# Performance work log

Measured on AMD Instinct MI355X. Metric: run time of the kernel, lower is better.

## Reference

```python
import jax, jax.numpy as jnp
import numpy as np

GAMMA = 0.01      # rbf gamma (init kwarg)
C = 10            # n_classes (len(nv))
NV = 500          # support vectors per class (equal segments)
# all (i, j) class pairs with i < j, in the original nested-loop order
PAIRS = np.array([(i, j) for i in range(C) for j in range(i + 1, C)], dtype=np.int32)
I_IDX = jnp.asarray(PAIRS[:, 0])  # [45]
J_IDX = jnp.asarray(PAIRS[:, 1])  # [45]


def setup_inputs() -> dict:
    key = jax.random.key(0)
    k1, k2, k3, k4 = jax.random.split(key, 4)
    x = jax.random.normal(k1, (8192, 256), dtype=jnp.float32)
    sv = jax.random.normal(k2, (5000, 256), dtype=jnp.float32)
    a = jax.random.normal(k3, (C - 1, 5000), dtype=jnp.float32) * 0.1  # dual coefs
    b = jax.random.normal(k4, (45,), dtype=jnp.float32) * 0.1          # intercepts per pair
    return {"x": x, "sv": sv, "a": a, "b": b}


def reference(x, sv, a, b):
    # RBF kernel matrix: k[n, s] = exp(-gamma * ||x_n - sv_s||^2)
    x_norm = jnp.sum(x * x, axis=1)[:, None]            # [N, 1]
    sv_norm = jnp.sum(sv * sv, axis=1)[None, :]         # [1, SV]
    k = jnp.exp(-GAMMA * (x_norm + sv_norm) + 2.0 * GAMMA * (x @ sv.T))  # [N, SV]

    N = x.shape[0]
    kr = k.reshape(N, C, NV)           # per-class SV segments
    ar = a.reshape(C - 1, C, NV)       # dual coef rows, segmented the same way
    # T[n, r, c] = sum_m a[r, segment c, m] * k[n, segment c, m]
    # (fuses every inner Python loop of the original into one contraction)
    T = jnp.einsum('ncm,rcm->nrc', kr, ar)              # [N, C-1, C]

    # decision for pair (i, j): a[i, seg j] . k_seg_j + a[j-1, seg i] . k_seg_i + b
    c = T[:, I_IDX, J_IDX] + T[:, J_IDX - 1, I_IDX] + b[None, :]  # [N, 45]

    # pairwise voting: winner i if c > 0 else j; class id = mode of votes
    votes = jnp.where(c > 0, I_IDX[None, :], J_IDX[None, :])      # [N, 45] int32
    counts = jnp.sum(jax.nn.one_hot(votes, C, dtype=jnp.float32), axis=1)  # [N, C]
    # argmax picks the smallest class index on ties, matching torch.mode
    class_ids = jnp.argmax(counts, axis=1).astype(jnp.int32)
    return (class_ids, class_ids)
```

## Files before the change

kernel.cpp:

```cpp
#include <hip/hip_runtime.h>
#include <hip/hip_fp16.h>
#include <cmath>


#define GAMMA 0.01f
constexpr int N  = 8192;
constexpr int D  = 256;
constexpr int S  = 5000;
constexpr int C  = 10;
constexpr int NV = 500;
constexpr int R  = 9;
constexpr int SPAD = 5120;

constexpr int ROW_BLOCKS = (N + S) / 4;
constexpr int A_BLOCKS   = (16 * SPAD) / 256;

typedef _Float16 f16x8 __attribute__((ext_vector_type(8)));
typedef _Float16 f16x4 __attribute__((ext_vector_type(4)));
typedef float    f32x4 __attribute__((ext_vector_type(4)));

__device__ __forceinline__ void gload16(const void* g, void* l) {
    __builtin_amdgcn_global_load_lds(
        (const __attribute__((address_space(1))) void*)g,
        (__attribute__((address_space(3))) void*)l, 16, 0, 0);
}

__global__ __launch_bounds__(256) void prep_kernel(const float* __restrict__ x,
                                                   const float* __restrict__ sv,
                                                   const float* __restrict__ a,
                                                   _Float16* __restrict__ xh,
                                                   _Float16* __restrict__ xl,
                                                   _Float16* __restrict__ sh,
                                                   _Float16* __restrict__ sl,
                                                   float* __restrict__ xn,
                                                   _Float16* __restrict__ ah,
                                                   _Float16* __restrict__ al,
                                                   float* __restrict__ svnp) {
    if (blockIdx.x >= ROW_BLOCKS) {
        int idx = (blockIdx.x - ROW_BLOCKS) * 256 + threadIdx.x;
        int r = idx / SPAD, col = idx - r * SPAD;
        int cls = col >> 9, j = col & 511;
        int s = cls * NV + ((j < NV) ? j : NV - 1);
        float av = (r < R && j < NV) ? a[(size_t)r * S + s] : 0.0f;
        _Float16 h = (_Float16)av;
        ah[idx] = h;
        al[idx] = (_Float16)((av - (float)h) * 4096.0f);
        return;
    }
    int gid  = blockIdx.x * blockDim.x + threadIdx.x;
    int wid  = gid >> 6;
    int lane = gid & 63;
    bool isx = wid < N;
    int  r   = isx ? wid : wid - N;
    const float* row = isx ? (x + (size_t)r * D) : (sv + (size_t)r * D);
    float4 v = reinterpret_cast<const float4*>(row)[lane];
    float s = v.x * v.x + v.y * v.y + v.z * v.z + v.w * v.w;
#pragma unroll
    for (int off = 32; off > 0; off >>= 1) s += __shfl_xor(s, off, 64);
    float vv[4] = {v.x, v.y, v.z, v.w};
    f16x4 h, l;
#pragma unroll
    for (int k = 0; k < 4; ++k) {
        _Float16 hi = (_Float16)vv[k];
        h[k] = hi;
        l[k] = (_Float16)((vv[k] - (float)hi) * 4096.0f);
    }
    size_t o = (size_t)r * D + lane * 4;
    *(f16x4*)((isx ? xh : sh) + o) = h;
    *(f16x4*)((isx ? xl : sl) + o) = l;
    if (lane == 0) {
        if (isx) {
            xn[r] = s;
        } else {
            int cls = r / NV, j = r - cls * NV;
            svnp[cls * 512 + j] = s;
            if (j == NV - 1)
                for (int p = NV; p < 512; ++p) svnp[cls * 512 + p] = s;
        }
    }
}

__global__ __launch_bounds__(256, 3) void svc_gemm(const _Float16* __restrict__ xh,
                                                   const _Float16* __restrict__ xl,
                                                   const _Float16* __restrict__ sh,
                                                   const _Float16* __restrict__ sl,
                                                   const _Float16* __restrict__ ahp,
                                                   const _Float16* __restrict__ alp,
                                                   const float* __restrict__ xnorm,
                                                   const float* __restrict__ svnp,
                                                   float* __restrict__ T) {
    __shared__ _Float16 SVs[2][2][128 * 32];
    __shared__ _Float16 Xs[2][2][64 * 32];

    const int tid  = threadIdx.x;
    const int n0   = blockIdx.x * 64;
    const int cls  = blockIdx.y;
    const int w    = tid >> 6;
    const int lane = tid & 63;
    const int wm   = w >> 1;
    const int wn   = w & 1;
    const int lx   = lane & 15;
    const int quad = lane >> 4;

    float xnr[2];
#pragma unroll
    for (int nt = 0; nt < 2; ++nt)
        xnr[nt] = xnorm[n0 + wn * 32 + nt * 16 + lx];

    int svoff[4], xoff[2];
#pragma unroll
    for (int mt = 0; mt < 4; ++mt) {
        int row = wm * 64 + mt * 16 + lx;
        svoff[mt] = row * 32 + ((quad - (row >> 1)) & 3) * 8;
    }
#pragma unroll
    for (int nt = 0; nt < 2; ++nt) {
        int row = wn * 32 + nt * 16 + lx;
        xoff[nt] = row * 32 + ((quad - (row >> 1)) & 3) * 8;
    }

    const int arow = tid >> 2, ag = tid & 3;
    const int sg   = (ag + (arow >> 1)) & 3;
    const int segend = cls * NV + NV - 1;
    const int ldsw = w * 512;

    auto stage = [&](int ph, int buf) {
        const int ch = ph >> 3, kb = ph & 7;
        const size_t koff = (size_t)(kb * 32 + sg * 8);
        const size_t goX  = (size_t)(n0 + arow) * D + koff;
        gload16(xh + goX, &Xs[buf][0][ldsw]);
        gload16(xl + goX, &Xs[buf][1][ldsw]);
        const int svbase = cls * NV + ch * 128;
        int svr0 = svbase + arow;      if (svr0 > segend) svr0 = segend;
        int svr1 = svbase + arow + 64; if (svr1 > segend) svr1 = segend;
        const size_t go0 = (size_t)svr0 * D + koff;
        const size_t go1 = (size_t)svr1 * D + koff;
        gload16(sh + go0, &SVs[buf][0][ldsw]);
        gload16(sl + go0, &SVs[buf][1][ldsw]);
        gload16(sh + go1, &SVs[buf][0][2048 + ldsw]);
        gload16(sl + go1, &SVs[buf][1][2048 + ldsw]);
    };

    f32x4 accM[4][2], accC[4][2];
#pragma unroll
    for (int mt = 0; mt < 4; ++mt)
#pragma unroll
        for (int nt = 0; nt < 2; ++nt) {
            accM[mt][nt] = (f32x4){0.f, 0.f, 0.f, 0.f};
            accC[mt][nt] = (f32x4){0.f, 0.f, 0.f, 0.f};
        }
    f32x4 accO[2], accOC[2];
#pragma unroll
    for (int nt = 0; nt < 2; ++nt) {
        accO[nt]  = (f32x4){0.f, 0.f, 0.f, 0.f};
        accOC[nt] = (f32x4){0.f, 0.f, 0.f, 0.f};
    }

    stage(0, 0);

    for (int ph = 0; ph < 32; ++ph) {
        const int buf = ph & 1;
        if (ph < 31) {
            stage(ph + 1, buf ^ 1);
            asm volatile("s_waitcnt vmcnt(6)" ::: "memory");
        } else {
            asm volatile("s_waitcnt vmcnt(0)" ::: "memory");
        }
        __builtin_amdgcn_s_barrier();
        asm volatile("" ::: "memory");

        f16x8 Am[2][4], Bx[2][2];
#pragma unroll
        for (int mt = 0; mt < 4; ++mt) {
            Am[0][mt] = *(const f16x8*)(&SVs[buf][0][svoff[mt]]);
            Am[1][mt] = *(const f16x8*)(&SVs[buf][1][svoff[mt]]);
        }
#pragma unroll
        for (int nt = 0; nt < 2; ++nt) {
            Bx[0][nt] = *(const f16x8*)(&Xs[buf][0][xoff[nt]]);
            Bx[1][nt] = *(const f16x8*)(&Xs[buf][1][xoff[nt]]);
        }
        __builtin_amdgcn_s_setprio(1);
#pragma unroll
        for (int mt = 0; mt < 4; ++mt)
#pragma unroll
            for (int nt = 0; nt < 2; ++nt) {
                accM[mt][nt] = __builtin_amdgcn_mfma_f32_16x16x32_f16(
                    Am[0][mt], Bx[0][nt], accM[mt][nt], 0, 0, 0);
                accC[mt][nt] = __builtin_amdgcn_mfma_f32_16x16x32_f16(
                    Am[0][mt], Bx[1][nt], accC[mt][nt], 0, 0, 0);
                accC[mt][nt] = __builtin_amdgcn_mfma_f32_16x16x32_f16(
                    Am[1][mt], Bx[0][nt], accC[mt][nt], 0, 0, 0);
            }
        __builtin_amdgcn_s_setprio(0);

        if ((ph & 7) == 7) {
            const int ch = ph >> 3;
            const int mbase = cls * 512 + ch * 128 + wm * 64;
#pragma unroll
            for (int mt = 0; mt < 4; ++mt) {
                const size_t ao = (size_t)lx * SPAD + mbase + mt * 16 + quad * 4;
                f16x4 afh = *(const f16x4*)(ahp + ao);
                f16x4 afl = *(const f16x4*)(alp + ao);
                float4 sn4 = *(const float4*)(svnp + mbase + mt * 16 + quad * 4);
#pragma unroll
                for (int nt = 0; nt < 2; ++nt) {
                    f16x4 bh, bl;
#pragma unroll
                    for (int reg = 0; reg < 4; ++reg) {
                        float dot = accM[mt][nt][reg]
                                  + accC[mt][nt][reg] * (1.0f / 4096.0f);
                        float e  = fmaf(2.0f * GAMMA, dot,
                                        -GAMMA * (xnr[nt] + sn4[reg]));
                        float kv = __expf(e);
                        _Float16 h = (_Float16)kv;
                        bh[reg] = h;
                        bl[reg] = (_Float16)((kv - (float)h) * 4096.0f);
                    }
                    accO[nt]  = __builtin_amdgcn_mfma_f32_16x16x16f16(
                        afh, bh, accO[nt], 0, 0, 0);
                    accOC[nt] = __builtin_amdgcn_mfma_f32_16x16x16f16(
                        afh, bl, accOC[nt], 0, 0, 0);
                    accOC[nt] = __builtin_amdgcn_mfma_f32_16x16x16f16(
                        afl, bh, accOC[nt], 0, 0, 0);
                    accM[mt][nt] = (f32x4){0.f, 0.f, 0.f, 0.f};
                    accC[mt][nt] = (f32x4){0.f, 0.f, 0.f, 0.f};
                }
            }
        }

        asm volatile("s_waitcnt lgkmcnt(0)" ::: "memory");
        __builtin_amdgcn_s_barrier();
        asm volatile("" ::: "memory");
    }

    float* scr = (float*)&SVs[0][0][0];
    if (wm == 0) {
#pragma unroll
        for (int nt = 0; nt < 2; ++nt)
#pragma unroll
            for (int reg = 0; reg < 4; ++reg) {
                int base = ((wn * 2 + nt) * 2) * 256 + (quad * 4 + reg) * 16 + lx;
                scr[base]       = accO[nt][reg];
                scr[base + 256] = accOC[nt][reg];
            }
    }
    __syncthreads();
    if (wm == 1) {
#pragma unroll
        for (int nt = 0; nt < 2; ++nt)
#pragma unroll
            for (int reg = 0; reg < 4; ++reg) {
                int r = quad * 4 + reg;
                if (r < R) {
                    int base = ((wn * 2 + nt) * 2) * 256 + r * 16 + lx;
                    float o  = accO[nt][reg]  + scr[base];
                    float oc = accOC[nt][reg] + scr[base + 256];
                    int n = n0 + wn * 32 + nt * 16 + lx;
                    T[(size_t)(r * 10 + cls) * N + n] = o + oc * (1.0f / 4096.0f);
                }
            }
    }
}

__global__ __launch_bounds__(256) void vote_kernel(const float* __restrict__ T,
                                                   const float* __restrict__ b,
                                                   int* __restrict__ out) {
    int n = blockIdx.x * blockDim.x + threadIdx.x;
    if (n >= N) return;
    float tv[90];
#pragma unroll
    for (int i = 0; i < 90; ++i) tv[i] = T[(size_t)i * N + n];
    int counts[C];
#pragma unroll
    for (int k = 0; k < C; ++k) counts[k] = 0;
    int p = 0;
#pragma unroll
    for (int i = 0; i < C; ++i) {
#pragma unroll
        for (int j = i + 1; j < C; ++j) {
            float c = tv[i * 10 + j] + tv[(j - 1) * 10 + i] + b[p];
            if (c > 0.f) counts[i]++; else counts[j]++;
            ++p;
        }
    }
    int best = 0;
#pragma unroll
    for (int k = 1; k < C; ++k)
        if (counts[k] > counts[best]) best = k;
    out[n]     = best;
    out[N + n] = best;
}

extern "C" void kernel_launch(void* const* d_in, const int* in_sizes, int n_in,
                              void* d_out, int out_size, void* d_ws, size_t ws_size,
                              hipStream_t stream) {
    const float* x  = (const float*)d_in[0];
    const float* sv = (const float*)d_in[1];
    const float* a  = (const float*)d_in[2];
    const float* b  = (const float*)d_in[3];
    int* out = (int*)d_out;

    char* wp = (char*)d_ws;
    _Float16* xh = (_Float16*)wp;  wp += (size_t)N * D * 2;
    _Float16* xl = (_Float16*)wp;  wp += (size_t)N * D * 2;
    _Float16* sh = (_Float16*)wp;  wp += (size_t)S * D * 2;
    _Float16* sl = (_Float16*)wp;  wp += (size_t)S * D * 2;
    float* xnorm  = (float*)wp;    wp += (size_t)N * 4;
    _Float16* ahp = (_Float16*)wp; wp += (size_t)16 * SPAD * 2;
    _Float16* alp = (_Float16*)wp; wp += (size_t)16 * SPAD * 2;
    float* svnp   = (float*)wp;    wp += (size_t)SPAD * 4;
    float* T      = (float*)wp;

    {
        prep_kernel<<<ROW_BLOCKS + A_BLOCKS, 256, 0, stream>>>(
            x, sv, a, xh, xl, sh, sl, xnorm, ahp, alp, svnp);
    }
    {
        dim3 grid(N / 64, C);
        svc_gemm<<<grid, 256, 0, stream>>>(xh, xl, sh, sl, ahp, alp,
                                           xnorm, svnp, T);
    }
    {
        vote_kernel<<<N / 256, 256, 0, stream>>>(T, b, out);
    }
}
```

Measured before the change: 164.6 us.

## Load X fragments directly into registers instead of staging through LDS

Removes the X tile from shared memory. Each wave now loads its own f16 hi/lo X fragments from global memory straight into registers, double-buffered across even and odd phases, while the SV tile still goes through LDS. The main loop is unrolled by two so each register buffer has a fixed name. This saves LDS traffic and capacity, which may allow more blocks per CU, but the two waves sharing an X slice now fetch it separately and the vmcnt accounting becomes more delicate.

```diff
diff --git a/kernel.cpp b/kernel.cpp
--- a/kernel.cpp
+++ b/kernel.cpp
@@ -90,7 +90,6 @@
                                                    const float* __restrict__ svnp,
                                                    float* __restrict__ T) {
     __shared__ _Float16 SVs[2][2][128 * 32];
-    __shared__ _Float16 Xs[2][2][64 * 32];
 
     const int tid  = threadIdx.x;
     const int n0   = blockIdx.x * 64;
@@ -107,16 +106,11 @@
     for (int nt = 0; nt < 2; ++nt)
         xnr[nt] = xnorm[n0 + wn * 32 + nt * 16 + lx];
 
-    int svoff[4], xoff[2];
+    int svoff[4];
 #pragma unroll
     for (int mt = 0; mt < 4; ++mt) {
         int row = wm * 64 + mt * 16 + lx;
         svoff[mt] = row * 32 + ((quad - (row >> 1)) & 3) * 8;
-    }
-#pragma unroll
-    for (int nt = 0; nt < 2; ++nt) {
-        int row = wn * 32 + nt * 16 + lx;
-        xoff[nt] = row * 32 + ((quad - (row >> 1)) & 3) * 8;
     }
 
     const int arow = tid >> 2, ag = tid & 3;
@@ -127,9 +121,6 @@
     auto stage = [&](int ph, int buf) {
         const int ch = ph >> 3, kb = ph & 7;
         const size_t koff = (size_t)(kb * 32 + sg * 8);
-        const size_t goX  = (size_t)(n0 + arow) * D + koff;
-        gload16(xh + goX, &Xs[buf][0][ldsw]);
-        gload16(xl + goX, &Xs[buf][1][ldsw]);
         const int svbase = cls * NV + ch * 128;
         int svr0 = svbase + arow;      if (svr0 > segend) svr0 = segend;
         int svr1 = svbase + arow + 64; if (svr1 > segend) svr1 = segend;
@@ -141,6 +132,18 @@
         gload16(sl + go1, &SVs[buf][1][2048 + ldsw]);
     };
 
+    const size_t xrow0 = (size_t)(n0 + wn * 32 + lx) * D + quad * 8;
+    const size_t xrow1 = (size_t)(n0 + wn * 32 + 16 + lx) * D + quad * 8;
+    f16x8 pBE[2][2], pBO[2][2];
+    auto loadB = [&](f16x8 (&dst)[2][2], int kb) {
+        const size_t o0 = xrow0 + kb * 32;
+        const size_t o1 = xrow1 + kb * 32;
+        dst[0][0] = *(const f16x8*)(xh + o0);
+        dst[1][0] = *(const f16x8*)(xl + o0);
+        dst[0][1] = *(const f16x8*)(xh + o1);
+        dst[1][1] = *(const f16x8*)(xl + o1);
+    };
+
     f32x4 accM[4][2], accC[4][2];
 #pragma unroll
     for (int mt = 0; mt < 4; ++mt)
@@ -156,79 +159,87 @@
         accOC[nt] = (f32x4){0.f, 0.f, 0.f, 0.f};
     }
 
-    stage(0, 0);
-
-    for (int ph = 0; ph < 32; ++ph) {
-        const int buf = ph & 1;
-        if (ph < 31) {
-            stage(ph + 1, buf ^ 1);
-            asm volatile("s_waitcnt vmcnt(6)" ::: "memory");
-        } else {
-            asm volatile("s_waitcnt vmcnt(0)" ::: "memory");
-        }
-        __builtin_amdgcn_s_barrier();
-        asm volatile("" ::: "memory");
-
-        f16x8 Am[2][4], Bx[2][2];
+    auto compute = [&](int buf, const f16x8 (&pB)[2][2]) {
+        f16x8 Am[2][4];
 #pragma unroll
         for (int mt = 0; mt < 4; ++mt) {
             Am[0][mt] = *(const f16x8*)(&SVs[buf][0][svoff[mt]]);
             Am[1][mt] = *(const f16x8*)(&SVs[buf][1][svoff[mt]]);
         }
-#pragma unroll
-        for (int nt = 0; nt < 2; ++nt) {
-            Bx[0][nt] = *(const f16x8*)(&Xs[buf][0][xoff[nt]]);
-            Bx[1][nt] = *(const f16x8*)(&Xs[buf][1][xoff[nt]]);
-        }
         __builtin_amdgcn_s_setprio(1);
 #pragma unroll
         for (int mt = 0; mt < 4; ++mt)
 #pragma unroll
             for (int nt = 0; nt < 2; ++nt) {
                 accM[mt][nt] = __builtin_amdgcn_mfma_f32_16x16x32_f16(
-                    Am[0][mt], Bx[0][nt], accM[mt][nt], 0, 0, 0);
+                    Am[0][mt], pB[0][nt], accM[mt][nt], 0, 0, 0);
                 accC[mt][nt] = __builtin_amdgcn_mfma_f32_16x16x32_f16(
-                    Am[0][mt], Bx[1][nt], accC[mt][nt], 0, 0, 0);
+                    Am[0][mt], pB[1][nt], accC[mt][nt], 0, 0, 0);
                 accC[mt][nt] = __builtin_amdgcn_mfma_f32_16x16x32_f16(
-                    Am[1][mt], Bx[0][nt], accC[mt][nt], 0, 0, 0);
+                    Am[1][mt], pB[0][nt], accC[mt][nt], 0, 0, 0);
             }
         __builtin_amdgcn_s_setprio(0);
-
-        if ((ph & 7) == 7) {
-            const int ch = ph >> 3;
-            const int mbase = cls * 512 + ch * 128 + wm * 64;
-#pragma unroll
-            for (int mt = 0; mt < 4; ++mt) {
-                const size_t ao = (size_t)lx * SPAD + mbase + mt * 16 + quad * 4;
-                f16x4 afh = *(const f16x4*)(ahp + ao);
-                f16x4 afl = *(const f16x4*)(alp + ao);
-                float4 sn4 = *(const float4*)(svnp + mbase + mt * 16 + quad * 4);
-#pragma unroll
-                for (int nt = 0; nt < 2; ++nt) {
-                    f16x4 bh, bl;
-#pragma unroll
-                    for (int reg = 0; reg < 4; ++reg) {
-                        float dot = accM[mt][nt][reg]
-                                  + accC[mt][nt][reg] * (1.0f / 4096.0f);
-                        float e  = fmaf(2.0f * GAMMA, dot,
-                                        -GAMMA * (xnr[nt] + sn4[reg]));
-                        float kv = __expf(e);
-                        _Float16 h = (_Float16)kv;
-                        bh[reg] = h;
-                        bl[reg] = (_Float16)((kv - (float)h) * 4096.0f);
-                    }
-                    accO[nt]  = __builtin_amdgcn_mfma_f32_16x16x16f16(
-                        afh, bh, accO[nt], 0, 0, 0);
-                    accOC[nt] = __builtin_amdgcn_mfma_f32_16x16x16f16(
-                        afh, bl, accOC[nt], 0, 0, 0);
-                    accOC[nt] = __builtin_amdgcn_mfma_f32_16x16x16f16(
-                        afl, bh, accOC[nt], 0, 0, 0);
-                    accM[mt][nt] = (f32x4){0.f, 0.f, 0.f, 0.f};
-                    accC[mt][nt] = (f32x4){0.f, 0.f, 0.f, 0.f};
+    };
+
+    auto epilogue = [&](int ch) {
+        const int mbase = cls * 512 + ch * 128 + wm * 64;
+#pragma unroll
+        for (int mt = 0; mt < 4; ++mt) {
+            const size_t ao = (size_t)lx * SPAD + mbase + mt * 16 + quad * 4;
+            f16x4 afh = *(const f16x4*)(ahp + ao);
+            f16x4 afl = *(const f16x4*)(alp + ao);
+            float4 sn4 = *(const float4*)(svnp + mbase + mt * 16 + quad * 4);
+#pragma unroll
+            for (int nt = 0; nt < 2; ++nt) {
+                f16x4 bh, bl;
+#pragma unroll
+                for (int reg = 0; reg < 4; ++reg) {
+                    float dot = accM[mt][nt][reg]
+                              + accC[mt][nt][reg] * (1.0f / 4096.0f);
+                    float e  = fmaf(2.0f * GAMMA, dot,
+                                    -GAMMA * (xnr[nt] + sn4[reg]));
+                    float kv = __expf(e);
+                    _Float16 h = (_Float16)kv;
+                    bh[reg] = h;
+                    bl[reg] = (_Float16)((kv - (float)h) * 4096.0f);
                 }
+                accO[nt]  = __builtin_amdgcn_mfma_f32_16x16x16f16(
+                    afh, bh, accO[nt], 0, 0, 0);
+                accOC[nt] = __builtin_amdgcn_mfma_f32_16x16x16f16(
+                    afh, bl, accOC[nt], 0, 0, 0);
+                accOC[nt] = __builtin_amdgcn_mfma_f32_16x16x16f16(
+                    afl, bh, accOC[nt], 0, 0, 0);
+                accM[mt][nt] = (f32x4){0.f, 0.f, 0.f, 0.f};
+                accC[mt][nt] = (f32x4){0.f, 0.f, 0.f, 0.f};
             }
         }
-
+    };
+
+    stage(0, 0);
+    loadB(pBE, 0);
+
+    for (int it = 0; it < 16; ++it) {
+        const int ph = it * 2;
+        stage(ph + 1, 1);
+        loadB(pBO, (ph + 1) & 7);
+        asm volatile("s_waitcnt vmcnt(8)" ::: "memory");
+        __builtin_amdgcn_s_barrier();
+        asm volatile("" ::: "memory");
+        compute(0, pBE);
+        asm volatile("s_waitcnt lgkmcnt(0)" ::: "memory");
+        __builtin_amdgcn_s_barrier();
+        asm volatile("" ::: "memory");
+        if (it < 15) {
+            stage(ph + 2, 0);
+            loadB(pBE, (ph + 2) & 7);
+            asm volatile("s_waitcnt vmcnt(8)" ::: "memory");
+        } else {
+            asm volatile("s_waitcnt vmcnt(0)" ::: "memory");
+        }
+        __builtin_amdgcn_s_barrier();
+        asm volatile("" ::: "memory");
+        compute(1, pBO);
+        if ((it & 3) == 3) epilogue(it >> 2);
         asm volatile("s_waitcnt lgkmcnt(0)" ::: "memory");
         __builtin_amdgcn_s_barrier();
         asm volatile("" ::: "memory");
```

Result: slower. 200.7 us (+21.9%).
